# Kernel optimization log

Hardware: AMD Instinct MI355X
Metric: run time of the kernel (lower is better)

## Reference

```python
import jax, jax.numpy as jnp
import numpy as np

N = 50000        # nodes
E = 600000       # edges (avg degree 12)
DIN = 128
DOUT = 128
ALPHA = 0.2      # leaky relu slope
C = 1.0          # curvature
SCALE = 10.0     # euclidean2poincare scale
EPS = 1e-15


def expmap0(u, c):
    # Poincare ball exponential map at the origin: tanh(sqrt(c)||u||) * u / (sqrt(c)||u||)
    sqrt_c = jnp.sqrt(c)
    norm = jnp.maximum(jnp.linalg.norm(u, axis=-1, keepdims=True), EPS)
    return jnp.tanh(sqrt_c * norm) * u / (sqrt_c * norm)


def setup_inputs() -> dict:
    key = jax.random.key(0)
    k1, k2, k3, k4 = jax.random.split(key, 4)
    x = jax.random.normal(k1, (N, DIN), dtype=jnp.float32)
    W = jax.random.normal(k2, (DIN, DOUT), dtype=jnp.float32) / np.sqrt(DIN)
    # xavier_normal with gain 1.414 on a (1, 2*DOUT) tensor
    a = jax.random.normal(k3, (2 * DOUT,), dtype=jnp.float32) * (1.414 * np.sqrt(2.0 / (1 + 2 * DOUT)))
    edge = jax.random.randint(k4, (2, E), 0, N, dtype=jnp.int32)
    return {"x": x, "W": W, "a": a, "edge": edge}


def reference(x, W, a, edge):
    # h = linear(input), no bias (use_bias=False)
    h = x @ W                                   # [N, DOUT]
    src, dst = edge[0], edge[1]
    h_src = h[src]                              # [E, DOUT] gather
    h_dst = h[dst]                              # [E, DOUT] gather
    # PoincareBall.concat of the two endpoint features -> [E, 2*DOUT]
    edge_h = jnp.concatenate([h_src, h_dst], axis=-1)
    logits = edge_h @ a                         # [E]
    edge_e = jnp.exp(-jax.nn.leaky_relu(logits, negative_slope=ALPHA))  # [E]
    # SpecialSpmm with b=ones -> per-row sum of edge values (row index = edge[0])
    e_rowsum = jax.ops.segment_sum(edge_e, src, num_segments=N)         # [N]
    # SpecialSpmm with b=h -> weighted scatter-sum aggregation
    h_prime = jax.ops.segment_sum(edge_e[:, None] * h_dst, src, num_segments=N)  # [N, DOUT]
    h_prime = h_prime / jnp.maximum(e_rowsum, EPS)[:, None]
    out = jax.nn.relu(h_prime)                  # activation
    out = expmap0(out / SCALE, C)               # euclidean2poincare(out, c, scale=10)
    return out
```

## Files before the change

### kernel.cpp

```cpp
#include <hip/hip_runtime.h>
#include <hip/hip_bf16.h>
#include <hip/hip_fp16.h>

#define DIN 128
#define DOUT 128
#define ALPHA 0.2f
#define EPS 1e-15f
#define INV_SCALE 0.1f
#define KB 16
#define CAP 64

typedef __attribute__((ext_vector_type(8))) unsigned short us8;

__device__ inline unsigned short f2b(float f) {
    unsigned int u = __float_as_uint(f);
    unsigned int r = (u + 0x7fffu + ((u >> 16) & 1u)) >> 16;
    return (unsigned short)r;
}
__device__ inline float blo(unsigned int v) { return __uint_as_float(v << 16); }
__device__ inline float bhi(unsigned int v) { return __uint_as_float(v & 0xffff0000u); }

__global__ __launch_bounds__(256) void gemm_s_kernel(
    const float* __restrict__ x, const float* __restrict__ W,
    const float* __restrict__ a, unsigned short* __restrict__ hb,
    float* __restrict__ s1, float* __restrict__ s2,
    int* __restrict__ cursor, int N)
{
    __shared__ float xT[128 * 64];
    __shared__ float Wc[2][KB * 128];
    const int t = threadIdx.x;
    const int row0 = blockIdx.x * 64;

    {
        int g0 = blockIdx.x * 256 + t;
        if (g0 < N) cursor[g0] = 0;
    }

#pragma unroll
    for (int it = 0; it < 8; ++it) {
        int idx = t + it * 256;
        int r = idx & 63;
        int k4 = idx >> 6;
        int row = row0 + r;
        float4 v = make_float4(0.f, 0.f, 0.f, 0.f);
        if (row < N) v = *(const float4*)(x + (size_t)row * DIN + k4 * 4);
        xT[(k4 * 4 + 0) * 64 + r] = v.x;
        xT[(k4 * 4 + 1) * 64 + r] = v.y;
        xT[(k4 * 4 + 2) * 64 + r] = v.z;
        xT[(k4 * 4 + 3) * 64 + r] = v.w;
    }

    auto stage = [&](int buf, int k0) {
        const float4* Wg = (const float4*)(W + k0 * 128);
        float4* Wd = (float4*)Wc[buf];
        Wd[t] = Wg[t];
        Wd[t + 256] = Wg[t + 256];
    };
    stage(0, 0);
    __syncthreads();

    const int cg = t & 15;
    const int rg = t >> 4;
    const int c0 = cg * 8;

    float acc[4][8];
#pragma unroll
    for (int i = 0; i < 4; ++i)
#pragma unroll
        for (int j = 0; j < 8; ++j) acc[i][j] = 0.f;

    const int NCH = 128 / KB;
    for (int c = 0; c < NCH; ++c) {
        if (c + 1 < NCH) stage((c + 1) & 1, (c + 1) * KB);
        const float* Wb = Wc[c & 1];
        const int kbase = c * KB;
#pragma unroll
        for (int kk = 0; kk < KB; ++kk) {
            float4 w0 = *(const float4*)(Wb + kk * 128 + c0);
            float4 w1 = *(const float4*)(Wb + kk * 128 + c0 + 4);
            float4 xv = *(const float4*)(xT + (kbase + kk) * 64 + rg * 4);
            float xr[4] = {xv.x, xv.y, xv.z, xv.w};
            float wr[8] = {w0.x, w0.y, w0.z, w0.w, w1.x, w1.y, w1.z, w1.w};
#pragma unroll
            for (int i = 0; i < 4; ++i)
#pragma unroll
                for (int j = 0; j < 8; ++j) acc[i][j] = fmaf(xr[i], wr[j], acc[i][j]);
        }
        __syncthreads();
    }

    float a1[8], a2[8];
#pragma unroll
    for (int j = 0; j < 8; ++j) {
        a1[j] = a[c0 + j];
        a2[j] = a[128 + c0 + j];
    }

#pragma unroll
    for (int ri = 0; ri < 4; ++ri) {
        int row = row0 + rg * 4 + ri;
        float p1 = 0.f, p2 = 0.f;
#pragma unroll
        for (int j = 0; j < 8; ++j) {
            p1 += acc[ri][j] * a1[j];
            p2 += acc[ri][j] * a2[j];
        }
#pragma unroll
        for (int m = 8; m >= 1; m >>= 1) {
            p1 += __shfl_xor(p1, m, 64);
            p2 += __shfl_xor(p2, m, 64);
        }
        if (row < N) {
            us8 hv;
#pragma unroll
            for (int j = 0; j < 8; ++j) hv[j] = f2b(acc[ri][j]);
            *(us8*)(hb + (size_t)row * DOUT + c0) = hv;
            if (cg == 0) { s1[row] = p1; s2[row] = p2; }
        }
    }
}

__global__ void scatter_kernel(
    const int* __restrict__ src, const int* __restrict__ dst,
    const float* __restrict__ s1, const float* __restrict__ s2,
    int* __restrict__ cursor, unsigned int* __restrict__ bucket, int E)
{
    int i = blockIdx.x * blockDim.x + threadIdx.x;
    int stride = gridDim.x * blockDim.x;
    for (; i < E; i += stride) {
        int s = src[i], d = dst[i];
        float logit = s1[s] + s2[d];
        float lr = (logit > 0.f) ? logit : ALPHA * logit;
        float wv = expf(-lr);
        unsigned int pk = ((unsigned int)__half_as_ushort(__float2half(wv)) << 16)
                        | (unsigned int)d;
        int pos = atomicAdd(&cursor[s], 1);
        if (pos < CAP) bucket[(size_t)s * CAP + pos] = pk;
    }
}

#define EDGE(k)                                                          \
    {                                                                    \
        float wf = __half2float(__ushort_as_half((unsigned short)(e##k >> 16))); \
        float wvs = wf * 0x1p24f;                                        \
        wsi += (long long)(int)wvs;                                      \
        axi += (long long)(int)(wvs * blo(v##k));                        \
        ayi += (long long)(int)(wvs * bhi(v##k));                        \
    }

__global__ __launch_bounds__(256) void aggregate_kernel(
    const unsigned int* __restrict__ hb, const int* __restrict__ cursor,
    const unsigned int* __restrict__ bucket, float* __restrict__ out, int N)
{
    const int node = blockIdx.x * 4 + (threadIdx.x >> 6);
    const int lane = threadIdx.x & 63;
    if (node >= N) return;

    const unsigned int* __restrict__ csr = bucket + (size_t)node * CAP;
    const int cnt = min(cursor[node], CAP);

    long long wsi = 0, axi = 0, ayi = 0;
    int i = 0;
    for (; i + 8 <= cnt; i += 8) {
        unsigned int e0 = csr[i + 0], e1 = csr[i + 1], e2 = csr[i + 2], e3 = csr[i + 3];
        unsigned int e4 = csr[i + 4], e5 = csr[i + 5], e6 = csr[i + 6], e7 = csr[i + 7];
        unsigned int v0 = hb[(size_t)(e0 & 0xffff) * 64 + lane];
        unsigned int v1 = hb[(size_t)(e1 & 0xffff) * 64 + lane];
        unsigned int v2 = hb[(size_t)(e2 & 0xffff) * 64 + lane];
        unsigned int v3 = hb[(size_t)(e3 & 0xffff) * 64 + lane];
        unsigned int v4 = hb[(size_t)(e4 & 0xffff) * 64 + lane];
        unsigned int v5 = hb[(size_t)(e5 & 0xffff) * 64 + lane];
        unsigned int v6 = hb[(size_t)(e6 & 0xffff) * 64 + lane];
        unsigned int v7 = hb[(size_t)(e7 & 0xffff) * 64 + lane];
        EDGE(0) EDGE(1) EDGE(2) EDGE(3) EDGE(4) EDGE(5) EDGE(6) EDGE(7)
    }
    for (; i + 2 <= cnt; i += 2) {
        unsigned int e0 = csr[i + 0], e1 = csr[i + 1];
        unsigned int v0 = hb[(size_t)(e0 & 0xffff) * 64 + lane];
        unsigned int v1 = hb[(size_t)(e1 & 0xffff) * 64 + lane];
        EDGE(0) EDGE(1)
    }
    if (i < cnt) {
        unsigned int e0 = csr[i];
        unsigned int v0 = hb[(size_t)(e0 & 0xffff) * 64 + lane];
        EDGE(0)
    }

    float ws = (float)wsi * 0x1p-24f;
    float ax = (float)axi * 0x1p-24f;
    float ay = (float)ayi * 0x1p-24f;

    float inv = 1.f / fmaxf(ws, EPS);
    float ux = fmaxf(ax * inv, 0.f) * INV_SCALE;
    float uy = fmaxf(ay * inv, 0.f) * INV_SCALE;

    float nsq = ux * ux + uy * uy;
#pragma unroll
    for (int m = 32; m >= 1; m >>= 1) nsq += __shfl_xor(nsq, m, 64);
    float norm = fmaxf(sqrtf(nsq), EPS);
    float scale = tanhf(norm) / norm;

    *(float2*)(out + (size_t)node * DOUT + lane * 2) = make_float2(ux * scale, uy * scale);
}

extern "C" void kernel_launch(void* const* d_in, const int* in_sizes, int n_in,
                              void* d_out, int out_size, void* d_ws, size_t ws_size,
                              hipStream_t stream)
{
    const float* x = (const float*)d_in[0];
    const float* W = (const float*)d_in[1];
    const float* a = (const float*)d_in[2];
    const int* edge = (const int*)d_in[3];
    const int N = in_sizes[0] / DIN;
    const int E = in_sizes[3] / 2;
    const int* src = edge;
    const int* dst = edge + E;
    float* out = (float*)d_out;

    char* w = (char*)d_ws;
    size_t off = 0;
    auto take = [&](size_t bytes) -> void* {
        void* p = (void*)(w + off);
        off += (bytes + 255) & ~(size_t)255;
        return p;
    };
    unsigned short* hb  = (unsigned short*)take((size_t)N * DOUT * 2);
    float*        s1     = (float*)       take((size_t)N * 4);
    float*        s2     = (float*)       take((size_t)N * 4);
    int*          cursor = (int*)         take((size_t)N * 4);
    unsigned int* bucket = (unsigned int*)take((size_t)N * CAP * 4);
    (void)ws_size; (void)n_in; (void)out_size;

    hipLaunchKernelGGL(gemm_s_kernel, dim3((N + 63) / 64), dim3(256), 0, stream,
                       x, W, a, hb, s1, s2, cursor, N);
    hipLaunchKernelGGL(scatter_kernel, dim3((E + 255) / 256), dim3(256), 0, stream,
                       src, dst, s1, s2, cursor, bucket, E);
    hipLaunchKernelGGL(aggregate_kernel, dim3((N + 3) / 4), dim3(256), 0, stream,
                       (const unsigned int*)hb, cursor, bucket, out, N);
}
```

Before: 108.7 us.

## Split GEMM into MFMA bf16 kernel plus precomputed W·a attention scores

Replaces the FP32 SIMT GEMM with a bf16 MFMA kernel. x is split into hi and lo bf16 parts for extra precision, while W is rounded to bf16. The attention scalars s1/s2 are computed separately as x·(W a), using a tiny kernel that folds a into W, so the logits keep fp32 precision. This removes the FP32 FMA bottleneck of the GEMM, at the cost of two extra launches and reading x twice. Rounding W to bf16 also changes the accuracy of h.

```diff
diff --git a/kernel.cpp b/kernel.cpp
--- a/kernel.cpp
+++ b/kernel.cpp
@@ -7,115 +7,157 @@
 #define ALPHA 0.2f
 #define EPS 1e-15f
 #define INV_SCALE 0.1f
-#define KB 16
 #define CAP 64
 
-typedef __attribute__((ext_vector_type(8))) unsigned short us8;
+typedef __attribute__((ext_vector_type(8))) short s8v;
+typedef __attribute__((ext_vector_type(4))) float f4v;
 
 __device__ inline unsigned short f2b(float f) {
     unsigned int u = __float_as_uint(f);
     unsigned int r = (u + 0x7fffu + ((u >> 16) & 1u)) >> 16;
     return (unsigned short)r;
 }
+__device__ inline float b2f(unsigned short u) { return __uint_as_float((unsigned int)u << 16); }
 __device__ inline float blo(unsigned int v) { return __uint_as_float(v << 16); }
 __device__ inline float bhi(unsigned int v) { return __uint_as_float(v & 0xffff0000u); }
 
-__global__ __launch_bounds__(256) void gemm_s_kernel(
-    const float* __restrict__ x, const float* __restrict__ W,
-    const float* __restrict__ a, unsigned short* __restrict__ hb,
+__global__ __launch_bounds__(256) void wa_kernel(
+    const float* __restrict__ W, const float* __restrict__ a,
+    float* __restrict__ wa)
+{
+    const int t = threadIdx.x;
+    const int k = t & 127;
+    const float* av = a + ((t >> 7) ? 128 : 0);
+    float s = 0.f;
+#pragma unroll 8
+    for (int c = 0; c < 128; ++c) s += W[k * 128 + c] * av[c];
+    wa[t] = s;
+}
+
+__global__ __launch_bounds__(256) void s1s2_kernel(
+    const float* __restrict__ x, const float* __restrict__ wa,
     float* __restrict__ s1, float* __restrict__ s2,
     int* __restrict__ cursor, int N)
 {
-    __shared__ float xT[128 * 64];
-    __shared__ float Wc[2][KB * 128];
     const int t = threadIdx.x;
-    const int row0 = blockIdx.x * 64;
-
     {
         int g0 = blockIdx.x * 256 + t;
         if (g0 < N) cursor[g0] = 0;
     }
-
-#pragma unroll
-    for (int it = 0; it < 8; ++it) {
-        int idx = t + it * 256;
-        int r = idx & 63;
-        int k4 = idx >> 6;
-        int row = row0 + r;
-        float4 v = make_float4(0.f, 0.f, 0.f, 0.f);
-        if (row < N) v = *(const float4*)(x + (size_t)row * DIN + k4 * 4);
-        xT[(k4 * 4 + 0) * 64 + r] = v.x;
-        xT[(k4 * 4 + 1) * 64 + r] = v.y;
-        xT[(k4 * 4 + 2) * 64 + r] = v.z;
-        xT[(k4 * 4 + 3) * 64 + r] = v.w;
-    }
-
-    auto stage = [&](int buf, int k0) {
-        const float4* Wg = (const float4*)(W + k0 * 128);
-        float4* Wd = (float4*)Wc[buf];
-        Wd[t] = Wg[t];
-        Wd[t + 256] = Wg[t + 256];
-    };
-    stage(0, 0);
+    const int row = blockIdx.x * 4 + (t >> 6);
+    const int l = t & 63;
+    if (row >= N) return;
+    float2 xv = *(const float2*)(x + (size_t)row * DIN + l * 2);
+    float2 w1 = *(const float2*)(wa + l * 2);
+    float2 w2 = *(const float2*)(wa + 128 + l * 2);
+    float p1 = xv.x * w1.x + xv.y * w1.y;
+    float p2 = xv.x * w2.x + xv.y * w2.y;
+#pragma unroll
+    for (int m = 32; m >= 1; m >>= 1) {
+        p1 += __shfl_xor(p1, m, 64);
+        p2 += __shfl_xor(p2, m, 64);
+    }
+    if (l == 0) { s1[row] = p1; s2[row] = p2; }
+}
+
+__global__ __launch_bounds__(256) void hb_kernel(
+    const float* __restrict__ x, const float* __restrict__ W,
+    unsigned short* __restrict__ hb, int N)
+{
+    __shared__ __align__(16) unsigned short xh[64 * 128];
+    __shared__ __align__(16) unsigned short xl[64 * 128];
+    __shared__ __align__(16) unsigned short wt[128 * 128];
+    const int t = threadIdx.x;
+    const int row0 = blockIdx.x * 64;
+
+#pragma unroll
+    for (int i = 0; i < 4; ++i) {
+        int idx = t + i * 256;
+        int r = idx >> 4;
+        int g = idx & 15;
+        int grow = row0 + r;
+        float v[8];
+        if (grow < N) {
+            const float4* xp = (const float4*)(x + (size_t)grow * DIN + g * 8);
+            float4 v0 = xp[0], v1 = xp[1];
+            v[0]=v0.x; v[1]=v0.y; v[2]=v0.z; v[3]=v0.w;
+            v[4]=v1.x; v[5]=v1.y; v[6]=v1.z; v[7]=v1.w;
+        } else {
+#pragma unroll
+            for (int j = 0; j < 8; ++j) v[j] = 0.f;
+        }
+        s8v hi, lo;
+#pragma unroll
+        for (int j = 0; j < 8; ++j) {
+            unsigned short h = f2b(v[j]);
+            hi[j] = (short)h;
+            lo[j] = (short)f2b(v[j] - b2f(h));
+        }
+        int gp = g ^ (r & 15);
+        *(s8v*)&xh[r * 128 + gp * 8] = hi;
+        *(s8v*)&xl[r * 128 + gp * 8] = lo;
+    }
+
+#pragma unroll
+    for (int i = 0; i < 8; ++i) {
+        int tau = t + i * 256;
+        int n = tau & 127;
+        int g = tau >> 7;
+        s8v wv;
+#pragma unroll
+        for (int j = 0; j < 8; ++j) {
+            float f = W[(size_t)(g * 8 + j) * DOUT + n];
+            wv[j] = (short)f2b(f);
+        }
+        int gp = g ^ (n & 15);
+        *(s8v*)&wt[n * 128 + gp * 8] = wv;
+    }
     __syncthreads();
 
-    const int cg = t & 15;
-    const int rg = t >> 4;
-    const int c0 = cg * 8;
-
-    float acc[4][8];
-#pragma unroll
-    for (int i = 0; i < 4; ++i)
-#pragma unroll
-        for (int j = 0; j < 8; ++j) acc[i][j] = 0.f;
-
-    const int NCH = 128 / KB;
-    for (int c = 0; c < NCH; ++c) {
-        if (c + 1 < NCH) stage((c + 1) & 1, (c + 1) * KB);
-        const float* Wb = Wc[c & 1];
-        const int kbase = c * KB;
-#pragma unroll
-        for (int kk = 0; kk < KB; ++kk) {
-            float4 w0 = *(const float4*)(Wb + kk * 128 + c0);
-            float4 w1 = *(const float4*)(Wb + kk * 128 + c0 + 4);
-            float4 xv = *(const float4*)(xT + (kbase + kk) * 64 + rg * 4);
-            float xr[4] = {xv.x, xv.y, xv.z, xv.w};
-            float wr[8] = {w0.x, w0.y, w0.z, w0.w, w1.x, w1.y, w1.z, w1.w};
-#pragma unroll
-            for (int i = 0; i < 4; ++i)
-#pragma unroll
-                for (int j = 0; j < 8; ++j) acc[i][j] = fmaf(xr[i], wr[j], acc[i][j]);
-        }
-        __syncthreads();
-    }
-
-    float a1[8], a2[8];
-#pragma unroll
-    for (int j = 0; j < 8; ++j) {
-        a1[j] = a[c0 + j];
-        a2[j] = a[128 + c0 + j];
-    }
-
-#pragma unroll
-    for (int ri = 0; ri < 4; ++ri) {
-        int row = row0 + rg * 4 + ri;
-        float p1 = 0.f, p2 = 0.f;
-#pragma unroll
-        for (int j = 0; j < 8; ++j) {
-            p1 += acc[ri][j] * a1[j];
-            p2 += acc[ri][j] * a2[j];
-        }
-#pragma unroll
-        for (int m = 8; m >= 1; m >>= 1) {
-            p1 += __shfl_xor(p1, m, 64);
-            p2 += __shfl_xor(p2, m, 64);
-        }
-        if (row < N) {
-            us8 hv;
-#pragma unroll
-            for (int j = 0; j < 8; ++j) hv[j] = f2b(acc[ri][j]);
-            *(us8*)(hb + (size_t)row * DOUT + c0) = hv;
-            if (cg == 0) { s1[row] = p1; s2[row] = p2; }
+    const int w = t >> 6;
+    const int l = t & 63;
+    const int l15 = l & 15;
+    const int lq = l >> 4;
+
+    f4v acc[4][2];
+#pragma unroll
+    for (int rt = 0; rt < 4; ++rt)
+#pragma unroll
+        for (int c = 0; c < 2; ++c) acc[rt][c] = (f4v)(0.f);
+
+#pragma unroll
+    for (int ks = 0; ks < 4; ++ks) {
+        int gp = (ks * 4 + lq) ^ l15;
+        s8v ah[4], al[4], bb[2];
+#pragma unroll
+        for (int rt = 0; rt < 4; ++rt) {
+            int row = rt * 16 + l15;
+            ah[rt] = *(const s8v*)&xh[row * 128 + gp * 8];
+            al[rt] = *(const s8v*)&xl[row * 128 + gp * 8];
+        }
+#pragma unroll
+        for (int c = 0; c < 2; ++c) {
+            int n = w * 32 + c * 16 + l15;
+            bb[c] = *(const s8v*)&wt[n * 128 + gp * 8];
+        }
+#pragma unroll
+        for (int rt = 0; rt < 4; ++rt)
+#pragma unroll
+            for (int c = 0; c < 2; ++c) {
+                acc[rt][c] = __builtin_amdgcn_mfma_f32_16x16x32_bf16(ah[rt], bb[c], acc[rt][c], 0, 0, 0);
+                acc[rt][c] = __builtin_amdgcn_mfma_f32_16x16x32_bf16(al[rt], bb[c], acc[rt][c], 0, 0, 0);
+            }
+    }
+
+#pragma unroll
+    for (int rt = 0; rt < 4; ++rt) {
+#pragma unroll
+        for (int r = 0; r < 4; ++r) {
+            int grow = row0 + rt * 16 + lq * 4 + r;
+            if (grow < N) {
+                hb[(size_t)grow * DOUT + w * 32 + l15]      = f2b(acc[rt][0][r]);
+                hb[(size_t)grow * DOUT + w * 32 + 16 + l15] = f2b(acc[rt][1][r]);
+            }
         }
     }
 }
@@ -227,12 +269,16 @@
     unsigned short* hb  = (unsigned short*)take((size_t)N * DOUT * 2);
     float*        s1     = (float*)       take((size_t)N * 4);
     float*        s2     = (float*)       take((size_t)N * 4);
+    float*        wa     = (float*)       take(256 * 4);
     int*          cursor = (int*)         take((size_t)N * 4);
     unsigned int* bucket = (unsigned int*)take((size_t)N * CAP * 4);
     (void)ws_size; (void)n_in; (void)out_size;
 
-    hipLaunchKernelGGL(gemm_s_kernel, dim3((N + 63) / 64), dim3(256), 0, stream,
-                       x, W, a, hb, s1, s2, cursor, N);
+    hipLaunchKernelGGL(wa_kernel, dim3(1), dim3(256), 0, stream, W, a, wa);
+    hipLaunchKernelGGL(s1s2_kernel, dim3((N + 3) / 4), dim3(256), 0, stream,
+                       x, wa, s1, s2, cursor, N);
+    hipLaunchKernelGGL(hb_kernel, dim3((N + 63) / 64), dim3(256), 0, stream,
+                       x, W, hb, N);
     hipLaunchKernelGGL(scatter_kernel, dim3((E + 255) / 256), dim3(256), 0, stream,
                        src, dst, s1, s2, cursor, bucket, E);
     hipLaunchKernelGGL(aggregate_kernel, dim3((N + 3) / 4), dim3(256), 0, stream,
```

Result: faster. 100.3 us (-7.7%).
